# Kernel optimization log

Measured on AMD Instinct MI355X. Metric: run time of the kernel, lower is better.

Reference implementation:

```python
import jax, jax.numpy as jnp
import numpy as np

BN_EPS = 1e-5
ATT_EPS = 1e-6


def _conv(x, w, groups=1):
    # x: [B,C,H,W], w: [O, C//groups, k, k], stride 1, SAME padding for odd k
    k = w.shape[-1]
    p = (k - 1) // 2
    return jax.lax.conv_general_dilated(
        x, w, window_strides=(1, 1), padding=[(p, p), (p, p)],
        dimension_numbers=('NCHW', 'OIHW', 'NCHW'), feature_group_count=groups)


def _bn(x, bnp):
    # bnp: [4, C] stacked (scale, bias, running_mean, running_var); eval-mode BN
    s, b, m, v = bnp[0], bnp[1], bnp[2], bnp[3]
    inv = s / jnp.sqrt(v + BN_EPS)
    return x * inv[None, :, None, None] + (b - m * inv)[None, :, None, None]


def _relu6(x):
    return jnp.clip(x, 0.0, 6.0)


def _ffn(x, fc1_w, fc1_bn, conv1_w, conv1_bn, conv2_w, conv2_bn, fc2_w, fc2_bn):
    # E_FFN: 1x1 ConvBNReLU6 -> dw5x5 ConvBNReLU6 & dw3x3 ConvBNReLU6 -> sum -> 1x1 ConvBN -> ReLU6
    C = x.shape[1]
    h = _relu6(_bn(_conv(x, fc1_w), fc1_bn))
    x1 = _relu6(_bn(_conv(h, conv1_w, groups=C), conv1_bn))
    x2 = _relu6(_bn(_conv(h, conv2_w, groups=C), conv2_bn))
    return _relu6(_bn(_conv(x1 + x2, fc2_w), fc2_bn))


def _bias(y, b):
    return y + b[None, :, None, None]


def setup_inputs() -> dict:
    key = jax.random.key(0)
    ks = jax.random.split(key, 16)
    C, M = 64, 8  # in_places, in_places // scale
    B, H, W = 4, 224, 224

    def w(k, shape, s=0.05):
        return (jax.random.normal(k, shape, dtype=jnp.float32) * s)

    def bn_params(k, c):
        k1, k2, k3, k4 = jax.random.split(k, 4)
        scale = 1.0 + 0.1 * jax.random.normal(k1, (c,), dtype=jnp.float32)
        bias = 0.1 * jax.random.normal(k2, (c,), dtype=jnp.float32)
        mean = 0.1 * jax.random.normal(k3, (c,), dtype=jnp.float32)
        var = 1.0 + 0.1 * jax.random.uniform(k4, (c,), dtype=jnp.float32)
        return jnp.stack([scale, bias, mean, var])  # [4, c]

    return {
        'x': jax.random.normal(ks[0], (B, C, H, W), dtype=jnp.float32),
        'gamma': jnp.full((1,), 0.5, dtype=jnp.float32),  # nonzero so attention branch matters
        'q_w': w(ks[1], (M, C, 1, 1)), 'q_b': w(ks[2], (M,)),
        'k_w': w(ks[3], (M, C, 1, 1)), 'k_b': w(ks[4], (M,)),
        'v_w': w(ks[5], (C, C, 1, 1)), 'v_b': w(ks[6], (C,)),
        'fc1_w': w(ks[7], (C, C, 1, 1)), 'fc1_bn': bn_params(ks[8], C),
        'conv1_w': w(ks[9], (C, 1, 5, 5)), 'conv1_bn': bn_params(ks[10], C),
        'conv2_w': w(ks[11], (C, 1, 3, 3)), 'conv2_bn': bn_params(ks[12], C),
        'fc2_w': w(ks[13], (C, C, 1, 1)), 'fc2_bn': bn_params(ks[14], C),
    }


def reference(x, gamma, q_w, q_b, k_w, k_b, v_w, v_b,
              fc1_w, fc1_bn, conv1_w, conv1_bn, conv2_w, conv2_bn, fc2_w, fc2_bn):
    B, C, H, W = x.shape
    N = H * W
    x_channel = _ffn(x, fc1_w, fc1_bn, conv1_w, conv1_bn, conv2_w, conv2_bn, fc2_w, fc2_bn)
    # softplus feature maps; Q,K: [B, m, N]
    Q = jax.nn.softplus(_bias(_conv(x, q_w), q_b).reshape(B, -1, N))
    K = jax.nn.softplus(_bias(_conv(x, k_w), k_b).reshape(B, -1, N))
    V = (_bias(_conv(x, v_w), v_b) + x_channel).reshape(B, C, N)
    Qt = jnp.swapaxes(Q, 1, 2)                              # [B, N, m]
    KV = jnp.einsum('bmn,bcn->bmc', K, V)                   # [B, m, C]
    norm = 1.0 / jnp.einsum('bnm,bm->bn', Qt, K.sum(-1) + ATT_EPS)  # [B, N]
    wv = jnp.einsum('bnm,bmc,bn->bcn', Qt, KV, norm).reshape(B, C, H, W)
    return x + gamma * wv
```

## Files before the change

kernel.cpp:

```cpp
#include <hip/hip_runtime.h>
#include <math.h>

#define B_ 4
#define C_ 64
#define M_ 8
#define H_ 224
#define W_ 224
#define N_ (H_*W_)
#define CN_ (C_*N_)
#define MN_ (M_*N_)
#define BCN_ (B_*CN_)
#define BMN_ (B_*MN_)
#define NPG_ 392

__device__ __forceinline__ float relu6f(float v){ return fminf(fmaxf(v,0.0f),6.0f); }
__device__ __forceinline__ float softplusf(float v){
  return v > 0.0f ? v + log1pf(expf(-v)) : log1pf(expf(v));
}

#define FMA4(A, W, X) { A.x = fmaf((W), (X).x, A.x); A.y = fmaf((W), (X).y, A.y); \
                        A.z = fmaf((W), (X).z, A.z); A.w = fmaf((W), (X).w, A.w); }

__global__ __launch_bounds__(256) void k_fc1k(const float* __restrict__ x,
                                              const float* __restrict__ w,
                                              const float* __restrict__ bn,
                                              const float* __restrict__ kw,
                                              const float* __restrict__ kb,
                                              float* __restrict__ h,
                                              float* __restrict__ Kq,
                                              float* __restrict__ ks_part)
{
  __shared__ float xsl[2*1024];
  __shared__ float wl [2*512];
  __shared__ float kt [512];
  const int tid  = threadIdx.x;
  const int b    = blockIdx.x / NPG_;
  const int pg   = blockIdx.x % NPG_;
  const int pix0 = pg*128;
  const float* xb = x + (size_t)b*CN_ + pix0;

  for (int idx = tid; idx < 512; idx += 256) {
    const int c = idx >> 3, m = idx & 7;
    kt[idx] = kw[m*64 + c];
  }

  const int scp = tid >> 5;
  const int spx = (tid & 31) << 2;
  const int e0 = tid*2, e1 = tid*2+1;
  const int wc0 = e0 >> 6, wo0 = e0 & 63;
  const int wc1 = e1 >> 6, wo1 = e1 & 63;

  {
    const float4 xr = *(const float4*)(xb + (size_t)scp*N_ + spx);
    const float w0r = w[wo0*64 + wc0];
    const float w1r = w[wo1*64 + wc1];
    *(float4*)&xsl[scp*128 + spx] = xr;
    wl[e0] = w0r; wl[e1] = w1r;
  }
  __syncthreads();

  const int lane = tid & 63, wv_ = tid >> 6;
  const int och  = 2*wv_ + (lane >> 5);
  const int ocb  = och*8;
  const int px4  = (lane & 31) << 2;

  float4 ah[8];
  float4 ak = {0,0,0,0};
  #pragma unroll
  for (int i = 0; i < 8; ++i) ah[i] = make_float4(0.f,0.f,0.f,0.f);

  for (int ck = 0; ck < 8; ++ck) {
    const int cur = ck & 1, nxt = cur ^ 1;
    const float* xc = &xsl[cur*1024];
    const float* wc = &wl[cur*512];
    float4 xr; float w0r, w1r;
    if (ck < 7) {
      const int c0n = (ck+1)*8;
      xr  = *(const float4*)(xb + (size_t)(c0n + scp)*N_ + spx);
      w0r = w[wo0*64 + c0n + wc0];
      w1r = w[wo1*64 + c0n + wc1];
    }
    #pragma unroll
    for (int cp = 0; cp < 8; ++cp) {
      const float4 xv = *(const float4*)&xc[cp*128 + px4];
      const float4 w0 = *(const float4*)&wc[cp*64 + ocb];
      const float4 w1 = *(const float4*)&wc[cp*64 + ocb + 4];
      const float kvw = kt[(ck*8+cp)*8 + och];
      FMA4(ah[0], w0.x, xv); FMA4(ah[1], w0.y, xv);
      FMA4(ah[2], w0.z, xv); FMA4(ah[3], w0.w, xv);
      FMA4(ah[4], w1.x, xv); FMA4(ah[5], w1.y, xv);
      FMA4(ah[6], w1.z, xv); FMA4(ah[7], w1.w, xv);
      FMA4(ak, kvw, xv);
    }
    if (ck < 7) {
      *(float4*)&xsl[nxt*1024 + scp*128 + spx] = xr;
      wl[nxt*512 + e0] = w0r; wl[nxt*512 + e1] = w1r;
    }
    __syncthreads();
  }

  float* hb = h + (size_t)b*CN_ + pix0 + px4;
  #pragma unroll
  for (int o = 0; o < 8; ++o) {
    const int oc = ocb + o;
    const float inv  = bn[oc] / sqrtf(bn[192+oc] + 1e-5f);
    const float beta = bn[64+oc] - bn[128+oc]*inv;
    float4 o4;
    o4.x = relu6f(fmaf(ah[o].x, inv, beta));
    o4.y = relu6f(fmaf(ah[o].y, inv, beta));
    o4.z = relu6f(fmaf(ah[o].z, inv, beta));
    o4.w = relu6f(fmaf(ah[o].w, inv, beta));
    *(float4*)(hb + (size_t)oc*N_) = o4;
  }
  {
    const float kbm = kb[och];
    float4 q;
    q.x = softplusf(ak.x + kbm); q.y = softplusf(ak.y + kbm);
    q.z = softplusf(ak.z + kbm); q.w = softplusf(ak.w + kbm);
    *(float4*)(Kq + (size_t)b*MN_ + (size_t)och*N_ + pix0 + px4) = q;
    float ss = (q.x + q.y) + (q.z + q.w);
    ss += __shfl_xor(ss, 1);
    ss += __shfl_xor(ss, 2);
    ss += __shfl_xor(ss, 4);
    ss += __shfl_xor(ss, 8);
    ss += __shfl_xor(ss, 16);
    if ((lane & 31) == 0)
      ks_part[(size_t)(b*NPG_ + pg)*8 + och] = ss;
  }
}

__global__ __launch_bounds__(256) void k_dw(const float* __restrict__ h,
                                            const float* __restrict__ w5,
                                            const float* __restrict__ w3,
                                            const float* __restrict__ bn1,
                                            const float* __restrict__ bn2,
                                            float* __restrict__ s)
{
  __shared__ float tile[36*37];
  const int tid = threadIdx.x;
  const int blk = blockIdx.x;
  const int t   = blk % 49;
  const int bc  = blk / 49;
  const int c   = bc & 63;
  const int tx0 = (t % 7) * 32;
  const int ty0 = (t / 7) * 32;
  const float* hb = h + (size_t)bc * N_;

  for (int idx = tid; idx < 1296; idx += 256) {
    const int ly = idx / 36, lx = idx - ly*36;
    const int gy = ty0 + ly - 2, gx = tx0 + lx - 2;
    float v = 0.0f;
    if (gy >= 0 && gy < H_ && gx >= 0 && gx < W_) v = hb[gy*W_ + gx];
    tile[ly*37 + lx] = v;
  }
  __syncthreads();

  float w5r[25], w3r[9];
  #pragma unroll
  for (int i = 0; i < 25; ++i) w5r[i] = w5[c*25 + i];
  #pragma unroll
  for (int i = 0; i < 9; ++i)  w3r[i] = w3[c*9 + i];
  const float inv1 = bn1[c] / sqrtf(bn1[192+c] + 1e-5f);
  const float bet1 = bn1[64+c] - bn1[128+c]*inv1;
  const float inv2 = bn2[c] / sqrtf(bn2[192+c] + 1e-5f);
  const float bet2 = bn2[64+c] - bn2[128+c]*inv2;

  const int ty  = tid >> 3;
  const int tx4 = (tid & 7) << 2;
  float a5[4] = {0,0,0,0}, a3[4] = {0,0,0,0};
  #pragma unroll
  for (int dy = 0; dy < 5; ++dy) {
    float r[8];
    #pragma unroll
    for (int i = 0; i < 8; ++i) r[i] = tile[(ty+dy)*37 + tx4 + i];
    #pragma unroll
    for (int dx = 0; dx < 5; ++dx) {
      const float wv = w5r[dy*5+dx];
      #pragma unroll
      for (int p = 0; p < 4; ++p) a5[p] = fmaf(wv, r[p+dx], a5[p]);
    }
    if (dy >= 1 && dy <= 3) {
      #pragma unroll
      for (int dx = 1; dx <= 3; ++dx) {
        const float wv = w3r[(dy-1)*3+(dx-1)];
        #pragma unroll
        for (int p = 0; p < 4; ++p) a3[p] = fmaf(wv, r[p+dx], a3[p]);
      }
    }
  }
  float* sb = s + (size_t)bc * N_ + (ty0+ty)*W_ + tx0 + tx4;
  float4 o4;
  o4.x = relu6f(fmaf(a5[0],inv1,bet1)) + relu6f(fmaf(a3[0],inv2,bet2));
  o4.y = relu6f(fmaf(a5[1],inv1,bet1)) + relu6f(fmaf(a3[1],inv2,bet2));
  o4.z = relu6f(fmaf(a5[2],inv1,bet1)) + relu6f(fmaf(a3[2],inv2,bet2));
  o4.w = relu6f(fmaf(a5[3],inv1,bet1)) + relu6f(fmaf(a3[3],inv2,bet2));
  *(float4*)sb = o4;
}

__global__ __launch_bounds__(256) void k_vkv(const float* __restrict__ x,
                                             const float* __restrict__ s,
                                             const float* __restrict__ vw,
                                             const float* __restrict__ vb,
                                             const float* __restrict__ fw,
                                             const float* __restrict__ fbn,
                                             const float* __restrict__ Kq,
                                             float* __restrict__ kv_part)
{
  __shared__ float xsl[2*1024];
  __shared__ float ssl[2*1024];
  __shared__ float wvl[2*512];
  __shared__ float wfl[2*512];
  const int tid  = threadIdx.x;
  const int b    = blockIdx.x / NPG_;
  const int pg   = blockIdx.x % NPG_;
  const int pix0 = pg*128;
  const float* xb = x + (size_t)b*CN_ + pix0;
  const float* sb = s + (size_t)b*CN_ + pix0;

  const int scp = tid >> 5;
  const int spx = (tid & 31) << 2;
  const int e0 = tid*2, e1 = tid*2+1;
  const int wc0 = e0 >> 6, wo0 = e0 & 63;
  const int wc1 = e1 >> 6, wo1 = e1 & 63;

  {
    const float4 xr = *(const float4*)(xb + (size_t)scp*N_ + spx);
    const float4 sr = *(const float4*)(sb + (size_t)scp*N_ + spx);
    const float a0 = vw[wo0*64 + wc0], a1 = vw[wo1*64 + wc1];
    const float f0 = fw[wo0*64 + wc0], f1 = fw[wo1*64 + wc1];
    *(float4*)&xsl[scp*128 + spx] = xr;
    *(float4*)&ssl[scp*128 + spx] = sr;
    wvl[e0] = a0; wvl[e1] = a1;
    wfl[e0] = f0; wfl[e1] = f1;
  }
  __syncthreads();

  const int lane = tid & 63, wv_ = tid >> 6;
  const int och  = 2*wv_ + (lane >> 5);
  const int ocb  = och*8;
  const int px4  = (lane & 31) << 2;

  float4 av[8], af[8];
  #pragma unroll
  for (int i = 0; i < 8; ++i) { av[i] = make_float4(0,0,0,0); af[i] = make_float4(0,0,0,0); }

  for (int ck = 0; ck < 8; ++ck) {
    const int cur = ck & 1, nxt = cur ^ 1;
    const float* xc = &xsl[cur*1024];
    const float* sc2 = &ssl[cur*1024];
    const float* wvc = &wvl[cur*512];
    const float* wfc = &wfl[cur*512];
    float4 xr, sr; float a0r, a1r, f0r, f1r;
    if (ck < 7) {
      const int c0n = (ck+1)*8;
      xr  = *(const float4*)(xb + (size_t)(c0n + scp)*N_ + spx);
      sr  = *(const float4*)(sb + (size_t)(c0n + scp)*N_ + spx);
      a0r = vw[wo0*64 + c0n + wc0]; a1r = vw[wo1*64 + c0n + wc1];
      f0r = fw[wo0*64 + c0n + wc0]; f1r = fw[wo1*64 + c0n + wc1];
    }
    #pragma unroll
    for (int cp = 0; cp < 8; ++cp) {
      const float4 xv = *(const float4*)&xc[cp*128 + px4];
      const float4 sv = *(const float4*)&sc2[cp*128 + px4];
      const float4 wa0 = *(const float4*)&wvc[cp*64 + ocb];
      const float4 wa1 = *(const float4*)&wvc[cp*64 + ocb + 4];
      const float4 wf0 = *(const float4*)&wfc[cp*64 + ocb];
      const float4 wf1 = *(const float4*)&wfc[cp*64 + ocb + 4];
      FMA4(av[0], wa0.x, xv); FMA4(av[1], wa0.y, xv);
      FMA4(av[2], wa0.z, xv); FMA4(av[3], wa0.w, xv);
      FMA4(av[4], wa1.x, xv); FMA4(av[5], wa1.y, xv);
      FMA4(av[6], wa1.z, xv); FMA4(av[7], wa1.w, xv);
      FMA4(af[0], wf0.x, sv); FMA4(af[1], wf0.y, sv);
      FMA4(af[2], wf0.z, sv); FMA4(af[3], wf0.w, sv);
      FMA4(af[4], wf1.x, sv); FMA4(af[5], wf1.y, sv);
      FMA4(af[6], wf1.z, sv); FMA4(af[7], wf1.w, sv);
    }
    if (ck < 7) {
      *(float4*)&xsl[nxt*1024 + scp*128 + spx] = xr;
      *(float4*)&ssl[nxt*1024 + scp*128 + spx] = sr;
      wvl[nxt*512 + e0] = a0r; wvl[nxt*512 + e1] = a1r;
      wfl[nxt*512 + e0] = f0r; wfl[nxt*512 + e1] = f1r;
    }
    __syncthreads();
  }

  float4 v4[8];
  #pragma unroll
  for (int o = 0; o < 8; ++o) {
    const int oc = ocb + o;
    const float inv  = fbn[oc] / sqrtf(fbn[192+oc] + 1e-5f);
    const float beta = fbn[64+oc] - fbn[128+oc]*inv;
    const float bias = vb[oc];
    v4[o].x = av[o].x + bias + relu6f(fmaf(af[o].x, inv, beta));
    v4[o].y = av[o].y + bias + relu6f(fmaf(af[o].y, inv, beta));
    v4[o].z = av[o].z + bias + relu6f(fmaf(af[o].z, inv, beta));
    v4[o].w = av[o].w + bias + relu6f(fmaf(af[o].w, inv, beta));
  }

  const float* Kb = Kq + (size_t)b*MN_ + pix0;
  for (int idx = tid; idx < 1024; idx += 256)
    xsl[idx] = Kb[(size_t)(idx >> 7)*N_ + (idx & 127)];
  __syncthreads();

  const int l31 = lane & 31;
  const int j   = 4*(l31 & 1) + 2*((l31 >> 1) & 1) + ((l31 >> 2) & 1);
  #pragma unroll
  for (int m = 0; m < 8; ++m) {
    const float4 kv4 = *(const float4*)&xsl[m*128 + px4];
    float p[8];
    #pragma unroll
    for (int o = 0; o < 8; ++o) {
      float t = kv4.x*v4[o].x;
      t = fmaf(kv4.y, v4[o].y, t);
      t = fmaf(kv4.z, v4[o].z, t);
      t = fmaf(kv4.w, v4[o].w, t);
      p[o] = t;
    }
    int nv = 8;
    #pragma unroll
    for (int mask = 1; mask <= 4; mask <<= 1) {
      nv >>= 1;
      const bool hi = (l31 & mask) != 0;
      #pragma unroll
      for (int i = 0; i < nv; ++i) {
        const float mine = hi ? p[i] : p[i+nv];
        const float th = __shfl_xor(mine, mask);
        p[i] = (hi ? p[i+nv] : p[i]) + th;
      }
    }
    p[0] += __shfl_xor(p[0], 8);
    p[0] += __shfl_xor(p[0], 16);
    if (l31 < 8) wvl[m*64 + ocb + j] = p[0];
  }
  __syncthreads();

  float* kp = kv_part + (size_t)(b*NPG_ + pg)*512;
  kp[tid]       = wvl[tid];
  kp[tid + 256] = wvl[tid + 256];
}

__global__ __launch_bounds__(256) void k_red(const float* __restrict__ kv_part,
                                             const float* __restrict__ ks_part,
                                             float* __restrict__ KV,
                                             float* __restrict__ Ksum)
{
  __shared__ float red[4][64];
  __shared__ float rks[256];
  const int blk = blockIdx.x;
  const int b = blk >> 3, seg = blk & 7;
  const int t = threadIdx.x;
  const int i = seg*64 + (t & 63);
  const int sl = t >> 6;
  const float* base = kv_part + (size_t)b*NPG_*512 + i;
  float a = 0.0f;
  for (int g = sl; g < NPG_; g += 4) a += base[(size_t)g*512];
  red[sl][t & 63] = a;
  __syncthreads();
  if (t < 64)
    KV[b*512 + seg*64 + t] = (red[0][t] + red[1][t]) + (red[2][t] + red[3][t]);

  if (seg == 0) {
    const int m = t & 7, g0 = t >> 3;
    float s2 = 0.0f;
    for (int g = g0; g < NPG_; g += 32)
      s2 += ks_part[(size_t)b*NPG_*8 + g*8 + m];
    rks[t] = s2;
    __syncthreads();
    if (t < 8) {
      float s3 = 0.0f;
      #pragma unroll
      for (int j2 = 0; j2 < 32; ++j2) s3 += rks[j2*8 + t];
      Ksum[b*8 + t] = s3;
    }
  }
}

__global__ __launch_bounds__(256) void k_out(const float* __restrict__ x,
                                             const float* __restrict__ qw,
                                             const float* __restrict__ qb,
                                             const float* __restrict__ gamma,
                                             const float* __restrict__ KV,
                                             const float* __restrict__ Ksum,
                                             float* __restrict__ out)
{
  __shared__ __align__(16) float kvt[64*8];
  __shared__ __align__(16) float wqt[64*8];
  __shared__ float ksl[8];
  const int tid = threadIdx.x;
  const int b  = blockIdx.x / 196;
  const int pg = blockIdx.x % 196;
  const int pix0 = pg*256;
  const float* xb = x + (size_t)b*CN_ + pix0 + tid;

  for (int idx = tid; idx < 512; idx += 256) {
    const int m = idx >> 6, c = idx & 63;
    kvt[c*8 + m] = KV[b*512 + idx];
    wqt[c*8 + m] = qw[idx];
  }
  if (tid < 8) ksl[tid] = Ksum[b*8 + tid] + 1e-6f;
  __syncthreads();

  float q[8] = {0,0,0,0,0,0,0,0};
  #pragma unroll 8
  for (int c = 0; c < 64; ++c) {
    const float xv = xb[(size_t)c*N_];
    const float4 w0 = *(const float4*)&wqt[c*8];
    const float4 w1 = *(const float4*)&wqt[c*8+4];
    q[0] = fmaf(w0.x, xv, q[0]);
    q[1] = fmaf(w0.y, xv, q[1]);
    q[2] = fmaf(w0.z, xv, q[2]);
    q[3] = fmaf(w0.w, xv, q[3]);
    q[4] = fmaf(w1.x, xv, q[4]);
    q[5] = fmaf(w1.y, xv, q[5]);
    q[6] = fmaf(w1.z, xv, q[6]);
    q[7] = fmaf(w1.w, xv, q[7]);
  }
  float den = 0.0f;
  #pragma unroll
  for (int m = 0; m < 8; ++m) {
    q[m] = softplusf(q[m] + qb[m]);
    den  = fmaf(q[m], ksl[m], den);
  }
  const float sc = gamma[0] / den;

  float* ob = out + (size_t)b*CN_ + pix0 + tid;
  #pragma unroll 8
  for (int c = 0; c < 64; ++c) {
    const float4 k0 = *(const float4*)&kvt[c*8];
    const float4 k1 = *(const float4*)&kvt[c*8+4];
    float wv;
    wv = q[0]*k0.x;
    wv = fmaf(q[1], k0.y, wv);
    wv = fmaf(q[2], k0.z, wv);
    wv = fmaf(q[3], k0.w, wv);
    wv = fmaf(q[4], k1.x, wv);
    wv = fmaf(q[5], k1.y, wv);
    wv = fmaf(q[6], k1.z, wv);
    wv = fmaf(q[7], k1.w, wv);
    ob[(size_t)c*N_] = fmaf(sc, wv, xb[(size_t)c*N_]);
  }
}

extern "C" void kernel_launch(void* const* d_in, const int* in_sizes, int n_in,
                              void* d_out, int out_size, void* d_ws, size_t ws_size,
                              hipStream_t stream) {
  const float* x      = (const float*)d_in[0];
  const float* gamma  = (const float*)d_in[1];
  const float* q_w    = (const float*)d_in[2];
  const float* q_b    = (const float*)d_in[3];
  const float* k_w    = (const float*)d_in[4];
  const float* k_b    = (const float*)d_in[5];
  const float* v_w    = (const float*)d_in[6];
  const float* v_b    = (const float*)d_in[7];
  const float* fc1_w  = (const float*)d_in[8];
  const float* fc1_bn = (const float*)d_in[9];
  const float* c1_w   = (const float*)d_in[10];
  const float* c1_bn  = (const float*)d_in[11];
  const float* c2_w   = (const float*)d_in[12];
  const float* c2_bn  = (const float*)d_in[13];
  const float* fc2_w  = (const float*)d_in[14];
  const float* fc2_bn = (const float*)d_in[15];
  float* outp = (float*)d_out;

  float* ws      = (float*)d_ws;
  float* bufA    = ws;
  float* bufS    = ws + (size_t)BCN_;
  float* bufK    = ws + (size_t)2*BCN_;
  float* ks_part = ws + (size_t)2*BCN_ + BMN_;
  float* kv      = ks_part + (size_t)B_*NPG_*8;
  float* ksum    = kv + 2048;
  float* kv_part = bufA;

  k_fc1k<<<dim3(B_*NPG_), dim3(256), 0, stream>>>(x, fc1_w, fc1_bn, k_w, k_b, bufA, bufK, ks_part);
  k_dw  <<<dim3(B_*C_*49), dim3(256), 0, stream>>>(bufA, c1_w, c2_w, c1_bn, c2_bn, bufS);
  k_vkv <<<dim3(B_*NPG_), dim3(256), 0, stream>>>(x, bufS, v_w, v_b, fc2_w, fc2_bn, bufK, kv_part);
  k_red <<<dim3(32), dim3(256), 0, stream>>>(kv_part, ks_part, kv, ksum);
  k_out <<<dim3(B_*196), dim3(256), 0, stream>>>(x, q_w, q_b, gamma, kv, ksum, outp);
}
```

Baseline: 332.6 us.

## Use bf16 MFMA for the 1x1 convolutions with channel-last bf16 activations

Adds a cast kernel that transposes x into a swizzled pixel-major bf16 layout. The fc1/K and V/fc2 1x1 convolutions are rewritten to use 16x16x32 bf16 MFMA instructions instead of scalar FP32 FMAs. The depthwise stage now writes its output as bf16 in the same swizzled channel-last layout, which halves that intermediate traffic. The aim is to cut VALU work and memory bandwidth, at the cost of bf16 precision loss and an extra cast pass over x.

```diff
diff --git a/kernel.cpp b/kernel.cpp
--- a/kernel.cpp
+++ b/kernel.cpp
@@ -12,16 +12,74 @@
 #define BCN_ (B_*CN_)
 #define BMN_ (B_*MN_)
 #define NPG_ 392
+#define NPG2_ 196
+
+typedef __attribute__((ext_vector_type(8))) short short8;
+typedef __attribute__((ext_vector_type(4))) float f32x4;
+typedef __attribute__((ext_vector_type(4))) unsigned int uint4v;
 
 __device__ __forceinline__ float relu6f(float v){ return fminf(fmaxf(v,0.0f),6.0f); }
 __device__ __forceinline__ float softplusf(float v){
   return v > 0.0f ? v + log1pf(expf(-v)) : log1pf(expf(v));
 }
-
-#define FMA4(A, W, X) { A.x = fmaf((W), (X).x, A.x); A.y = fmaf((W), (X).y, A.y); \
-                        A.z = fmaf((W), (X).z, A.z); A.w = fmaf((W), (X).w, A.w); }
-
-__global__ __launch_bounds__(256) void k_fc1k(const float* __restrict__ x,
+__device__ __forceinline__ unsigned short f2bf(float f){
+  unsigned int u = __float_as_uint(f);
+  u += 0x7FFFu + ((u >> 16) & 1u);
+  return (unsigned short)(u >> 16);
+}
+__device__ __forceinline__ short8 pack8(float4 a, float4 b){
+  unsigned int p0,p1,p2,p3;
+  asm("v_cvt_pk_bf16_f32 %0, %1, %2" : "=v"(p0) : "v"(a.x), "v"(a.y));
+  asm("v_cvt_pk_bf16_f32 %0, %1, %2" : "=v"(p1) : "v"(a.z), "v"(a.w));
+  asm("v_cvt_pk_bf16_f32 %0, %1, %2" : "=v"(p2) : "v"(b.x), "v"(b.y));
+  asm("v_cvt_pk_bf16_f32 %0, %1, %2" : "=v"(p3) : "v"(b.z), "v"(b.w));
+  uint4v q = {p0,p1,p2,p3};
+  return __builtin_bit_cast(short8, q);
+}
+
+__global__ __launch_bounds__(256) void k_cast(const float* __restrict__ x,
+                                              unsigned short* __restrict__ xt)
+{
+  __shared__ float t[64*65];
+  const int tid = threadIdx.x;
+  const int b  = blockIdx.x / 784;
+  const int pg = blockIdx.x % 784;
+  const int px0 = pg*64;
+  const float* xb = x + (size_t)b*CN_ + px0;
+  #pragma unroll
+  for (int r = 0; r < 4; ++r) {
+    const int c  = (tid>>4) + 16*r;
+    const int p4 = (tid&15)<<2;
+    const float4 v = *(const float4*)(xb + (size_t)c*N_ + p4);
+    float* d = &t[c*65 + p4];
+    d[0]=v.x; d[1]=v.y; d[2]=v.z; d[3]=v.w;
+  }
+  __syncthreads();
+  const int px = tid & 63;
+  const int swz = px & 7;
+  unsigned short* ob = xt + ((size_t)b*N_ + px0 + px)*64;
+  #pragma unroll
+  for (int gg = 0; gg < 2; ++gg) {
+    const int cg = ((tid>>6)<<1) + gg;
+    const int c0 = cg<<3;
+    unsigned int rr0,rr1,rr2,rr3;
+    {
+      const float* tc = &t[px];
+      const float a0 = tc[(c0+0)*65], a1 = tc[(c0+1)*65];
+      const float a2 = tc[(c0+2)*65], a3 = tc[(c0+3)*65];
+      const float a4 = tc[(c0+4)*65], a5 = tc[(c0+5)*65];
+      const float a6 = tc[(c0+6)*65], a7 = tc[(c0+7)*65];
+      asm("v_cvt_pk_bf16_f32 %0, %1, %2" : "=v"(rr0) : "v"(a0), "v"(a1));
+      asm("v_cvt_pk_bf16_f32 %0, %1, %2" : "=v"(rr1) : "v"(a2), "v"(a3));
+      asm("v_cvt_pk_bf16_f32 %0, %1, %2" : "=v"(rr2) : "v"(a4), "v"(a5));
+      asm("v_cvt_pk_bf16_f32 %0, %1, %2" : "=v"(rr3) : "v"(a6), "v"(a7));
+    }
+    uint4v q = {rr0,rr1,rr2,rr3};
+    *(uint4v*)(ob + ((cg ^ swz)<<3)) = q;
+  }
+}
+
+__global__ __launch_bounds__(256) void k_fc1m(const unsigned short* __restrict__ xt,
                                               const float* __restrict__ w,
                                               const float* __restrict__ bn,
                                               const float* __restrict__ kw,
@@ -30,103 +88,107 @@
                                               float* __restrict__ Kq,
                                               float* __restrict__ ks_part)
 {
-  __shared__ float xsl[2*1024];
-  __shared__ float wl [2*512];
-  __shared__ float kt [512];
-  const int tid  = threadIdx.x;
-  const int b    = blockIdx.x / NPG_;
-  const int pg   = blockIdx.x % NPG_;
-  const int pix0 = pg*128;
-  const float* xb = x + (size_t)b*CN_ + pix0;
-
-  for (int idx = tid; idx < 512; idx += 256) {
-    const int c = idx >> 3, m = idx & 7;
-    kt[idx] = kw[m*64 + c];
-  }
-
-  const int scp = tid >> 5;
-  const int spx = (tid & 31) << 2;
-  const int e0 = tid*2, e1 = tid*2+1;
-  const int wc0 = e0 >> 6, wo0 = e0 & 63;
-  const int wc1 = e1 >> 6, wo1 = e1 & 63;
+  __shared__ unsigned short xl[256*64];
+  __shared__ float invb[2][64];
+  __shared__ float ksl[4][8];
+  const int tid = threadIdx.x;
+  const int b   = blockIdx.x / NPG2_;
+  const int pg  = blockIdx.x % NPG2_;
+  const int pix0 = pg*256;
 
   {
-    const float4 xr = *(const float4*)(xb + (size_t)scp*N_ + spx);
-    const float w0r = w[wo0*64 + wc0];
-    const float w1r = w[wo1*64 + wc1];
-    *(float4*)&xsl[scp*128 + spx] = xr;
-    wl[e0] = w0r; wl[e1] = w1r;
-  }
-  __syncthreads();
-
-  const int lane = tid & 63, wv_ = tid >> 6;
-  const int och  = 2*wv_ + (lane >> 5);
-  const int ocb  = och*8;
-  const int px4  = (lane & 31) << 2;
-
-  float4 ah[8];
-  float4 ak = {0,0,0,0};
-  #pragma unroll
-  for (int i = 0; i < 8; ++i) ah[i] = make_float4(0.f,0.f,0.f,0.f);
-
-  for (int ck = 0; ck < 8; ++ck) {
-    const int cur = ck & 1, nxt = cur ^ 1;
-    const float* xc = &xsl[cur*1024];
-    const float* wc = &wl[cur*512];
-    float4 xr; float w0r, w1r;
-    if (ck < 7) {
-      const int c0n = (ck+1)*8;
-      xr  = *(const float4*)(xb + (size_t)(c0n + scp)*N_ + spx);
-      w0r = w[wo0*64 + c0n + wc0];
-      w1r = w[wo1*64 + c0n + wc1];
-    }
-    #pragma unroll
-    for (int cp = 0; cp < 8; ++cp) {
-      const float4 xv = *(const float4*)&xc[cp*128 + px4];
-      const float4 w0 = *(const float4*)&wc[cp*64 + ocb];
-      const float4 w1 = *(const float4*)&wc[cp*64 + ocb + 4];
-      const float kvw = kt[(ck*8+cp)*8 + och];
-      FMA4(ah[0], w0.x, xv); FMA4(ah[1], w0.y, xv);
-      FMA4(ah[2], w0.z, xv); FMA4(ah[3], w0.w, xv);
-      FMA4(ah[4], w1.x, xv); FMA4(ah[5], w1.y, xv);
-      FMA4(ah[6], w1.z, xv); FMA4(ah[7], w1.w, xv);
-      FMA4(ak, kvw, xv);
-    }
-    if (ck < 7) {
-      *(float4*)&xsl[nxt*1024 + scp*128 + spx] = xr;
-      wl[nxt*512 + e0] = w0r; wl[nxt*512 + e1] = w1r;
-    }
-    __syncthreads();
-  }
-
-  float* hb = h + (size_t)b*CN_ + pix0 + px4;
-  #pragma unroll
-  for (int o = 0; o < 8; ++o) {
-    const int oc = ocb + o;
-    const float inv  = bn[oc] / sqrtf(bn[192+oc] + 1e-5f);
-    const float beta = bn[64+oc] - bn[128+oc]*inv;
-    float4 o4;
-    o4.x = relu6f(fmaf(ah[o].x, inv, beta));
-    o4.y = relu6f(fmaf(ah[o].y, inv, beta));
-    o4.z = relu6f(fmaf(ah[o].z, inv, beta));
-    o4.w = relu6f(fmaf(ah[o].w, inv, beta));
-    *(float4*)(hb + (size_t)oc*N_) = o4;
-  }
-  {
-    const float kbm = kb[och];
-    float4 q;
-    q.x = softplusf(ak.x + kbm); q.y = softplusf(ak.y + kbm);
-    q.z = softplusf(ak.z + kbm); q.w = softplusf(ak.w + kbm);
-    *(float4*)(Kq + (size_t)b*MN_ + (size_t)och*N_ + pix0 + px4) = q;
-    float ss = (q.x + q.y) + (q.z + q.w);
-    ss += __shfl_xor(ss, 1);
-    ss += __shfl_xor(ss, 2);
-    ss += __shfl_xor(ss, 4);
-    ss += __shfl_xor(ss, 8);
-    ss += __shfl_xor(ss, 16);
-    if ((lane & 31) == 0)
-      ks_part[(size_t)(b*NPG_ + pg)*8 + och] = ss;
-  }
+    const uint4v* src = (const uint4v*)(xt + ((size_t)b*N_ + pix0)*64);
+    uint4v* dst = (uint4v*)xl;
+    #pragma unroll
+    for (int r = 0; r < 8; ++r) dst[r*256 + tid] = src[r*256 + tid];
+  }
+  if (tid < 64) {
+    const float inv = bn[tid] / sqrtf(bn[192+tid] + 1e-5f);
+    invb[0][tid] = inv;
+    invb[1][tid] = bn[64+tid] - bn[128+tid]*inv;
+  }
+  const int lane = tid & 63, wv = tid >> 6;
+  const int l15 = lane & 15, u = lane >> 4;
+
+  short8 aw[5][2];
+  #pragma unroll
+  for (int t = 0; t < 5; ++t) {
+    #pragma unroll
+    for (int kk = 0; kk < 2; ++kk) {
+      const int c0 = kk*32 + u*8;
+      float4 f0 = {0,0,0,0}, f1 = {0,0,0,0};
+      if (t < 4) {
+        const float* wr = w + (t*16 + l15)*64 + c0;
+        f0 = *(const float4*)wr; f1 = *(const float4*)(wr+4);
+      } else if (l15 < 8) {
+        const float* wr = kw + l15*64 + c0;
+        f0 = *(const float4*)wr; f1 = *(const float4*)(wr+4);
+      }
+      aw[t][kk] = pack8(f0, f1);
+    }
+  }
+  __syncthreads();
+
+  f32x4 acc[5][4];
+  #pragma unroll
+  for (int t = 0; t < 5; ++t)
+    #pragma unroll
+    for (int s = 0; s < 4; ++s) acc[t][s] = (f32x4){0.f,0.f,0.f,0.f};
+
+  const int pxw = wv*64;
+  #pragma unroll
+  for (int kk = 0; kk < 2; ++kk) {
+    #pragma unroll
+    for (int s = 0; s < 4; ++s) {
+      const int pxl = pxw + s*16 + l15;
+      const short8 bx = *(const short8*)(xl + pxl*64 + (((kk*4+u) ^ (pxl&7))<<3));
+      #pragma unroll
+      for (int t = 0; t < 5; ++t)
+        acc[t][s] = __builtin_amdgcn_mfma_f32_16x16x32_bf16(aw[t][kk], bx, acc[t][s], 0, 0, 0);
+    }
+  }
+
+  float* hb = h + (size_t)b*CN_;
+  #pragma unroll
+  for (int t = 0; t < 4; ++t) {
+    #pragma unroll
+    for (int s = 0; s < 4; ++s) {
+      const int px = pix0 + pxw + s*16 + l15;
+      #pragma unroll
+      for (int r = 0; r < 4; ++r) {
+        const int oc = t*16 + u*4 + r;
+        hb[(size_t)oc*N_ + px] = relu6f(fmaf(acc[t][s][r], invb[0][oc], invb[1][oc]));
+      }
+    }
+  }
+  float ksr[4] = {0.f,0.f,0.f,0.f};
+  if (u < 2) {
+    #pragma unroll
+    for (int s = 0; s < 4; ++s) {
+      const int px = pix0 + pxw + s*16 + l15;
+      #pragma unroll
+      for (int r = 0; r < 4; ++r) {
+        const int m = u*4 + r;
+        const float kq = softplusf(acc[4][s][r] + kb[m]);
+        Kq[(size_t)b*MN_ + (size_t)m*N_ + px] = kq;
+        ksr[r] += kq;
+      }
+    }
+  }
+  #pragma unroll
+  for (int r = 0; r < 4; ++r) {
+    float v = ksr[r];
+    v += __shfl_xor(v, 1); v += __shfl_xor(v, 2);
+    v += __shfl_xor(v, 4); v += __shfl_xor(v, 8);
+    ksr[r] = v;
+  }
+  if (l15 == 0 && u < 2) {
+    #pragma unroll
+    for (int r = 0; r < 4; ++r) ksl[wv][u*4+r] = ksr[r];
+  }
+  __syncthreads();
+  if (tid < 8)
+    ks_part[(size_t)blockIdx.x*8 + tid] = (ksl[0][tid]+ksl[1][tid]) + (ksl[2][tid]+ksl[3][tid]);
 }
 
 __global__ __launch_bounds__(256) void k_dw(const float* __restrict__ h,
@@ -134,7 +196,7 @@
                                             const float* __restrict__ w3,
                                             const float* __restrict__ bn1,
                                             const float* __restrict__ bn2,
-                                            float* __restrict__ s)
+                                            unsigned short* __restrict__ st)
 {
   __shared__ float tile[36*37];
   const int tid = threadIdx.x;
@@ -188,17 +250,22 @@
       }
     }
   }
-  float* sb = s + (size_t)bc * N_ + (ty0+ty)*W_ + tx0 + tx4;
-  float4 o4;
-  o4.x = relu6f(fmaf(a5[0],inv1,bet1)) + relu6f(fmaf(a3[0],inv2,bet2));
-  o4.y = relu6f(fmaf(a5[1],inv1,bet1)) + relu6f(fmaf(a3[1],inv2,bet2));
-  o4.z = relu6f(fmaf(a5[2],inv1,bet1)) + relu6f(fmaf(a3[2],inv2,bet2));
-  o4.w = relu6f(fmaf(a5[3],inv1,bet1)) + relu6f(fmaf(a3[3],inv2,bet2));
-  *(float4*)sb = o4;
-}
-
-__global__ __launch_bounds__(256) void k_vkv(const float* __restrict__ x,
-                                             const float* __restrict__ s,
+  const int b = bc >> 6;
+  const int pxr = tx0 + tx4;
+  const int pxg = (ty0+ty)*W_ + pxr;
+  unsigned short* ob = st + ((size_t)b*N_ + pxg)*64;
+  float o[4];
+  o[0] = relu6f(fmaf(a5[0],inv1,bet1)) + relu6f(fmaf(a3[0],inv2,bet2));
+  o[1] = relu6f(fmaf(a5[1],inv1,bet1)) + relu6f(fmaf(a3[1],inv2,bet2));
+  o[2] = relu6f(fmaf(a5[2],inv1,bet1)) + relu6f(fmaf(a3[2],inv2,bet2));
+  o[3] = relu6f(fmaf(a5[3],inv1,bet1)) + relu6f(fmaf(a3[3],inv2,bet2));
+  #pragma unroll
+  for (int p = 0; p < 4; ++p)
+    ob[(size_t)p*64 + (c ^ (((pxr+p)&7)<<3))] = f2bf(o[p]);
+}
+
+__global__ __launch_bounds__(256) void k_vkm(const unsigned short* __restrict__ xt,
+                                             const unsigned short* __restrict__ st,
                                              const float* __restrict__ vw,
                                              const float* __restrict__ vb,
                                              const float* __restrict__ fw,
@@ -206,137 +273,123 @@
                                              const float* __restrict__ Kq,
                                              float* __restrict__ kv_part)
 {
-  __shared__ float xsl[2*1024];
-  __shared__ float ssl[2*1024];
-  __shared__ float wvl[2*512];
-  __shared__ float wfl[2*512];
-  const int tid  = threadIdx.x;
-  const int b    = blockIdx.x / NPG_;
-  const int pg   = blockIdx.x % NPG_;
+  __shared__ unsigned short xl[128*64];
+  __shared__ unsigned short sl[128*64];
+  __shared__ float kl[8*128];
+  __shared__ float invb[3][64];
+  __shared__ float kvw[4][512];
+  const int tid = threadIdx.x;
+  const int b   = blockIdx.x / NPG_;
+  const int pg  = blockIdx.x % NPG_;
   const int pix0 = pg*128;
-  const float* xb = x + (size_t)b*CN_ + pix0;
-  const float* sb = s + (size_t)b*CN_ + pix0;
-
-  const int scp = tid >> 5;
-  const int spx = (tid & 31) << 2;
-  const int e0 = tid*2, e1 = tid*2+1;
-  const int wc0 = e0 >> 6, wo0 = e0 & 63;
-  const int wc1 = e1 >> 6, wo1 = e1 & 63;
 
   {
-    const float4 xr = *(const float4*)(xb + (size_t)scp*N_ + spx);
-    const float4 sr = *(const float4*)(sb + (size_t)scp*N_ + spx);
-    const float a0 = vw[wo0*64 + wc0], a1 = vw[wo1*64 + wc1];
-    const float f0 = fw[wo0*64 + wc0], f1 = fw[wo1*64 + wc1];
-    *(float4*)&xsl[scp*128 + spx] = xr;
-    *(float4*)&ssl[scp*128 + spx] = sr;
-    wvl[e0] = a0; wvl[e1] = a1;
-    wfl[e0] = f0; wfl[e1] = f1;
-  }
-  __syncthreads();
-
-  const int lane = tid & 63, wv_ = tid >> 6;
-  const int och  = 2*wv_ + (lane >> 5);
-  const int ocb  = och*8;
-  const int px4  = (lane & 31) << 2;
-
-  float4 av[8], af[8];
-  #pragma unroll
-  for (int i = 0; i < 8; ++i) { av[i] = make_float4(0,0,0,0); af[i] = make_float4(0,0,0,0); }
-
-  for (int ck = 0; ck < 8; ++ck) {
-    const int cur = ck & 1, nxt = cur ^ 1;
-    const float* xc = &xsl[cur*1024];
-    const float* sc2 = &ssl[cur*1024];
-    const float* wvc = &wvl[cur*512];
-    const float* wfc = &wfl[cur*512];
-    float4 xr, sr; float a0r, a1r, f0r, f1r;
-    if (ck < 7) {
-      const int c0n = (ck+1)*8;
-      xr  = *(const float4*)(xb + (size_t)(c0n + scp)*N_ + spx);
-      sr  = *(const float4*)(sb + (size_t)(c0n + scp)*N_ + spx);
-      a0r = vw[wo0*64 + c0n + wc0]; a1r = vw[wo1*64 + c0n + wc1];
-      f0r = fw[wo0*64 + c0n + wc0]; f1r = fw[wo1*64 + c0n + wc1];
-    }
-    #pragma unroll
-    for (int cp = 0; cp < 8; ++cp) {
-      const float4 xv = *(const float4*)&xc[cp*128 + px4];
-      const float4 sv = *(const float4*)&sc2[cp*128 + px4];
-      const float4 wa0 = *(const float4*)&wvc[cp*64 + ocb];
-      const float4 wa1 = *(const float4*)&wvc[cp*64 + ocb + 4];
-      const float4 wf0 = *(const float4*)&wfc[cp*64 + ocb];
-      const float4 wf1 = *(const float4*)&wfc[cp*64 + ocb + 4];
-      FMA4(av[0], wa0.x, xv); FMA4(av[1], wa0.y, xv);
-      FMA4(av[2], wa0.z, xv); FMA4(av[3], wa0.w, xv);
-      FMA4(av[4], wa1.x, xv); FMA4(av[5], wa1.y, xv);
-      FMA4(av[6], wa1.z, xv); FMA4(av[7], wa1.w, xv);
-      FMA4(af[0], wf0.x, sv); FMA4(af[1], wf0.y, sv);
-      FMA4(af[2], wf0.z, sv); FMA4(af[3], wf0.w, sv);
-      FMA4(af[4], wf1.x, sv); FMA4(af[5], wf1.y, sv);
-      FMA4(af[6], wf1.z, sv); FMA4(af[7], wf1.w, sv);
-    }
-    if (ck < 7) {
-      *(float4*)&xsl[nxt*1024 + scp*128 + spx] = xr;
-      *(float4*)&ssl[nxt*1024 + scp*128 + spx] = sr;
-      wvl[nxt*512 + e0] = a0r; wvl[nxt*512 + e1] = a1r;
-      wfl[nxt*512 + e0] = f0r; wfl[nxt*512 + e1] = f1r;
-    }
-    __syncthreads();
-  }
-
-  float4 v4[8];
-  #pragma unroll
-  for (int o = 0; o < 8; ++o) {
-    const int oc = ocb + o;
-    const float inv  = fbn[oc] / sqrtf(fbn[192+oc] + 1e-5f);
-    const float beta = fbn[64+oc] - fbn[128+oc]*inv;
-    const float bias = vb[oc];
-    v4[o].x = av[o].x + bias + relu6f(fmaf(af[o].x, inv, beta));
-    v4[o].y = av[o].y + bias + relu6f(fmaf(af[o].y, inv, beta));
-    v4[o].z = av[o].z + bias + relu6f(fmaf(af[o].z, inv, beta));
-    v4[o].w = av[o].w + bias + relu6f(fmaf(af[o].w, inv, beta));
-  }
-
-  const float* Kb = Kq + (size_t)b*MN_ + pix0;
-  for (int idx = tid; idx < 1024; idx += 256)
-    xsl[idx] = Kb[(size_t)(idx >> 7)*N_ + (idx & 127)];
-  __syncthreads();
-
-  const int l31 = lane & 31;
-  const int j   = 4*(l31 & 1) + 2*((l31 >> 1) & 1) + ((l31 >> 2) & 1);
+    const size_t gb = ((size_t)b*N_ + pix0)*64;
+    const uint4v* sx = (const uint4v*)(xt + gb);
+    const uint4v* ss = (const uint4v*)(st + gb);
+    uint4v* dx = (uint4v*)xl;
+    uint4v* ds = (uint4v*)sl;
+    #pragma unroll
+    for (int r = 0; r < 4; ++r) {
+      dx[r*256 + tid] = sx[r*256 + tid];
+      ds[r*256 + tid] = ss[r*256 + tid];
+    }
+    const float* Kb = Kq + (size_t)b*MN_ + pix0;
+    #pragma unroll
+    for (int r = 0; r < 4; ++r) {
+      const int idx = r*256 + tid;
+      kl[idx] = Kb[(size_t)(idx>>7)*N_ + (idx&127)];
+    }
+  }
+  if (tid < 64) {
+    const float inv = fbn[tid] / sqrtf(fbn[192+tid] + 1e-5f);
+    invb[0][tid] = inv;
+    invb[1][tid] = fbn[64+tid] - fbn[128+tid]*inv;
+    invb[2][tid] = vb[tid];
+  }
+  const int lane = tid & 63, wv = tid >> 6;
+  const int l15 = lane & 15, u = lane >> 4;
+
+  short8 awv[4][2], awf[4][2];
+  #pragma unroll
+  for (int t = 0; t < 4; ++t) {
+    #pragma unroll
+    for (int kk = 0; kk < 2; ++kk) {
+      const int roff = (t*16 + l15)*64 + kk*32 + u*8;
+      awv[t][kk] = pack8(*(const float4*)(vw + roff), *(const float4*)(vw + roff + 4));
+      awf[t][kk] = pack8(*(const float4*)(fw + roff), *(const float4*)(fw + roff + 4));
+    }
+  }
+  __syncthreads();
+
+  f32x4 av[4][2], af[4][2];
+  #pragma unroll
+  for (int t = 0; t < 4; ++t)
+    #pragma unroll
+    for (int s = 0; s < 2; ++s) { av[t][s] = (f32x4){0.f,0.f,0.f,0.f}; af[t][s] = (f32x4){0.f,0.f,0.f,0.f}; }
+
+  const int pxw = wv*32;
+  #pragma unroll
+  for (int kk = 0; kk < 2; ++kk) {
+    #pragma unroll
+    for (int s = 0; s < 2; ++s) {
+      const int pxl = pxw + s*16 + l15;
+      const int off = pxl*64 + (((kk*4+u) ^ (pxl&7))<<3);
+      const short8 bx = *(const short8*)(xl + off);
+      const short8 bs = *(const short8*)(sl + off);
+      #pragma unroll
+      for (int t = 0; t < 4; ++t) {
+        av[t][s] = __builtin_amdgcn_mfma_f32_16x16x32_bf16(awv[t][kk], bx, av[t][s], 0, 0, 0);
+        af[t][s] = __builtin_amdgcn_mfma_f32_16x16x32_bf16(awf[t][kk], bs, af[t][s], 0, 0, 0);
+      }
+    }
+  }
+
+  #pragma unroll
+  for (int t = 0; t < 4; ++t) {
+    #pragma unroll
+    for (int s = 0; s < 2; ++s) {
+      #pragma unroll
+      for (int r = 0; r < 4; ++r) {
+        const int oc = t*16 + u*4 + r;
+        av[t][s][r] = av[t][s][r] + invb[2][oc]
+                    + relu6f(fmaf(af[t][s][r], invb[0][oc], invb[1][oc]));
+      }
+    }
+  }
+
+  const int jrev = 8*(l15&1) + 4*((l15>>1)&1) + 2*((l15>>2)&1) + ((l15>>3)&1);
+  const int cdst = (jrev>>2)*16 + u*4 + (jrev&3);
   #pragma unroll
   for (int m = 0; m < 8; ++m) {
-    const float4 kv4 = *(const float4*)&xsl[m*128 + px4];
-    float p[8];
-    #pragma unroll
-    for (int o = 0; o < 8; ++o) {
-      float t = kv4.x*v4[o].x;
-      t = fmaf(kv4.y, v4[o].y, t);
-      t = fmaf(kv4.z, v4[o].z, t);
-      t = fmaf(kv4.w, v4[o].w, t);
-      p[o] = t;
-    }
-    int nv = 8;
-    #pragma unroll
-    for (int mask = 1; mask <= 4; mask <<= 1) {
+    const float k0 = kl[m*128 + pxw + l15];
+    const float k1 = kl[m*128 + pxw + 16 + l15];
+    float p[16];
+    #pragma unroll
+    for (int t = 0; t < 4; ++t)
+      #pragma unroll
+      for (int r = 0; r < 4; ++r)
+        p[t*4+r] = fmaf(k0, av[t][0][r], k1 * av[t][1][r]);
+    int nv = 16;
+    #pragma unroll
+    for (int mask = 1; mask <= 8; mask <<= 1) {
       nv >>= 1;
-      const bool hi = (l31 & mask) != 0;
-      #pragma unroll
-      for (int i = 0; i < nv; ++i) {
-        const float mine = hi ? p[i] : p[i+nv];
-        const float th = __shfl_xor(mine, mask);
-        p[i] = (hi ? p[i+nv] : p[i]) + th;
-      }
-    }
-    p[0] += __shfl_xor(p[0], 8);
-    p[0] += __shfl_xor(p[0], 16);
-    if (l31 < 8) wvl[m*64 + ocb + j] = p[0];
-  }
-  __syncthreads();
-
+      const bool hi = (l15 & mask) != 0;
+      #pragma unroll
+      for (int i = 0; i < 8; ++i) {
+        if (i < nv) {
+          const float mine = hi ? p[i] : p[i+nv];
+          const float th = __shfl_xor(mine, mask);
+          p[i] = (hi ? p[i+nv] : p[i]) + th;
+        }
+      }
+    }
+    kvw[wv][m*64 + cdst] = p[0];
+  }
+  __syncthreads();
   float* kp = kv_part + (size_t)(b*NPG_ + pg)*512;
-  kp[tid]       = wvl[tid];
-  kp[tid + 256] = wvl[tid + 256];
+  kp[tid]       = (kvw[0][tid]+kvw[1][tid]) + (kvw[2][tid]+kvw[3][tid]);
+  kp[tid+256]   = (kvw[0][tid+256]+kvw[1][tid+256]) + (kvw[2][tid+256]+kvw[3][tid+256]);
 }
 
 __global__ __launch_bounds__(256) void k_red(const float* __restrict__ kv_part,
@@ -362,8 +415,8 @@
   if (seg == 0) {
     const int m = t & 7, g0 = t >> 3;
     float s2 = 0.0f;
-    for (int g = g0; g < NPG_; g += 32)
-      s2 += ks_part[(size_t)b*NPG_*8 + g*8 + m];
+    for (int g = g0; g < NPG2_; g += 32)
+      s2 += ks_part[(size_t)b*NPG2_*8 + g*8 + m];
     rks[t] = s2;
     __syncthreads();
     if (t < 8) {
@@ -387,8 +440,8 @@
   __shared__ __align__(16) float wqt[64*8];
   __shared__ float ksl[8];
   const int tid = threadIdx.x;
-  const int b  = blockIdx.x / 196;
-  const int pg = blockIdx.x % 196;
+  const int b  = blockIdx.x / NPG2_;
+  const int pg = blockIdx.x % NPG2_;
   const int pix0 = pg*256;
   const float* xb = x + (size_t)b*CN_ + pix0 + tid;
 
@@ -462,18 +515,20 @@
   const float* fc2_bn = (const float*)d_in[15];
   float* outp = (float*)d_out;
 
-  float* ws      = (float*)d_ws;
-  float* bufA    = ws;
-  float* bufS    = ws + (size_t)BCN_;
-  float* bufK    = ws + (size_t)2*BCN_;
-  float* ks_part = ws + (size_t)2*BCN_ + BMN_;
-  float* kv      = ks_part + (size_t)B_*NPG_*8;
-  float* ksum    = kv + 2048;
-  float* kv_part = bufA;
-
-  k_fc1k<<<dim3(B_*NPG_), dim3(256), 0, stream>>>(x, fc1_w, fc1_bn, k_w, k_b, bufA, bufK, ks_part);
-  k_dw  <<<dim3(B_*C_*49), dim3(256), 0, stream>>>(bufA, c1_w, c2_w, c1_bn, c2_bn, bufS);
-  k_vkv <<<dim3(B_*NPG_), dim3(256), 0, stream>>>(x, bufS, v_w, v_b, fc2_w, fc2_bn, bufK, kv_part);
+  float* ws = (float*)d_ws;
+  float* h            = ws;
+  unsigned short* xt  = (unsigned short*)(ws + (size_t)BCN_);
+  unsigned short* st  = xt + (size_t)BCN_;
+  float* Kq           = ws + (size_t)2*BCN_;
+  float* ks_part      = ws + (size_t)2*BCN_ + BMN_;
+  float* kv           = ks_part + (size_t)B_*NPG2_*8;
+  float* ksum         = kv + 2048;
+  float* kv_part      = h;
+
+  k_cast<<<dim3(B_*784), dim3(256), 0, stream>>>(x, xt);
+  k_fc1m<<<dim3(B_*NPG2_), dim3(256), 0, stream>>>(xt, fc1_w, fc1_bn, k_w, k_b, h, Kq, ks_part);
+  k_dw  <<<dim3(B_*C_*49), dim3(256), 0, stream>>>(h, c1_w, c2_w, c1_bn, c2_bn, st);
+  k_vkm <<<dim3(B_*NPG_), dim3(256), 0, stream>>>(xt, st, v_w, v_b, fc2_w, fc2_bn, Kq, kv_part);
   k_red <<<dim3(32), dim3(256), 0, stream>>>(kv_part, ks_part, kv, ksum);
-  k_out <<<dim3(B_*196), dim3(256), 0, stream>>>(x, q_w, q_b, gamma, kv, ksum, outp);
-}
+  k_out <<<dim3(B_*NPG2_), dim3(256), 0, stream>>>(x, q_w, q_b, gamma, kv, ksum, outp);
+}
```

After: 567.1 us. 70.5% more time.
